# Performance work log

Measured on AMD Instinct MI355X. Metric: run time of the kernel, lower is better.

The kernel has to match this reference:

```python
import jax, jax.numpy as jnp
import numpy as np

N_NODES = 50000
N_EDGES = 800000
IN_DIM, HID_DIM, OUT_DIM, N_HEADS = 256, 256, 64, 4

def setup_inputs() -> dict:
    key = jax.random.key(0)
    ks = jax.random.split(key, 8)
    x = jax.random.normal(ks[0], (N_NODES, IN_DIM), dtype=jnp.float32)
    idx = jax.random.randint(ks[1], (2, N_EDGES), 0, N_NODES, dtype=jnp.int64)
    elem = jax.random.uniform(ks[2], (N_EDGES,), dtype=jnp.float32)
    # MLP params (2 layers: in->hid, hid->out), one set per head; small scale for stability
    W1 = jax.random.normal(ks[3], (N_HEADS, IN_DIM, HID_DIM), dtype=jnp.float32) * 0.05
    b1 = jnp.zeros((N_HEADS, HID_DIM), dtype=jnp.float32)
    W2 = jax.random.normal(ks[4], (N_HEADS, HID_DIM, OUT_DIM), dtype=jnp.float32) * 0.05
    b2 = jnp.zeros((N_HEADS, OUT_DIM), dtype=jnp.float32)
    # Attention: Linear(2*out+1 -> 1)
    attn_w = jax.random.normal(ks[5], (N_HEADS, 2 * OUT_DIM + 1, 1), dtype=jnp.float32) * 0.05
    attn_b = jnp.zeros((N_HEADS, 1), dtype=jnp.float32)
    return {"x": x, "idx": idx, "elem": elem, "W1": W1, "b1": b1,
            "W2": W2, "b2": b2, "attn_w": attn_w, "attn_b": attn_b}

def reference(x, idx, elem, W1, b1, W2, b2, attn_w, attn_b):
    n = x.shape[0]
    src, dst = idx[0], idx[1]

    def head(W1h, b1h, W2h, b2h, awh, abh):
        # 2-layer MLP on node features: [N, out]
        feats = jnp.maximum(x @ W1h + b1h, 0.0) @ W2h + b2h
        f_src = feats[src]            # [E, out]
        f_dst = feats[dst]            # [E, out]
        x_cat = jnp.concatenate([f_src, f_dst, elem[:, None]], axis=1)  # [E, 2*out+1]
        score = (x_cat @ awh + abh)[:, 0]                # [E]
        w = jnp.exp(score - jnp.max(score))              # globally-shifted exp, as in source
        # SpecialSpmm: sparse [N,N] (rows=src, cols=dst, vals=w) @ dense
        pooled = jax.ops.segment_sum(w[:, None] * f_dst, src, num_segments=n)  # [N, out]
        row_sum = jax.ops.segment_sum(w, src, num_segments=n)                  # [N]
        return pooled / row_sum[:, None]

    h = jax.vmap(head)(W1, b1, W2, b2, attn_w, attn_b)   # [H, N, out]
    return jnp.transpose(h, (1, 0, 2)).reshape(n, -1)    # cat heads -> [N, H*out]
```

## Files before the change

kernel.cpp:

```cpp
#include <hip/hip_runtime.h>
#include <math.h>


#define N_HEADS 4
#define IN_DIM 256
#define HID_DIM 256
#define OUT_DIM 64
#define ATT_STRIDE (2 * OUT_DIM + 1)
#define LDSP 264

typedef __attribute__((ext_vector_type(8))) short bf16x8;
typedef __attribute__((ext_vector_type(4))) float f32x4;

__device__ __forceinline__ unsigned short bf16rne(float f) {
  unsigned int u = __float_as_uint(f);
  u += 0x7fffu + ((u >> 16) & 1u);
  return (unsigned short)(u >> 16);
}


#define W1N (N_HEADS * IN_DIM * HID_DIM)
#define W2N (N_HEADS * HID_DIM * OUT_DIM)

__global__ __launch_bounds__(256) void convw_kernel(const float* __restrict__ W1,
                                                    const float* __restrict__ W2,
                                                    unsigned short* __restrict__ W1T,
                                                    unsigned short* __restrict__ W2T) {
  int id = blockIdx.x * 256 + threadIdx.x;
  if (id < W1N) {
    int k = id & 255, j = (id >> 8) & 255, h = id >> 16;
    W1T[id] = bf16rne(W1[((size_t)h * 256 + k) * 256 + j]);
  } else if (id < W1N + W2N) {
    int t = id - W1N;
    int k = t & 255, d = (t >> 8) & 63, h = t >> 14;
    W2T[t] = bf16rne(W2[((size_t)h * 256 + k) * 64 + d]);
  }
}


__global__ __launch_bounds__(256) void count_kernel(const int* __restrict__ src,
                                                    int* __restrict__ cnt, int E) {
  int e = blockIdx.x * 256 + threadIdx.x;
  if (e < E) atomicAdd(&cnt[src[e]], 1);
}

__global__ __launch_bounds__(1024) void scan_kernel(const int* __restrict__ cnt,
                                                    int* __restrict__ offs, int N) {
  __shared__ int part[1024];
  int t = threadIdx.x;
  int chunk = (N + 1023) >> 10;
  int s0 = t * chunk;
  int s1e = min(s0 + chunk, N);
  int sum = 0;
  for (int i = s0; i < s1e; ++i) sum += cnt[i];
  part[t] = sum;
  __syncthreads();
  for (int off = 1; off < 1024; off <<= 1) {
    int v = (t >= off) ? part[t - off] : 0;
    __syncthreads();
    part[t] += v;
    __syncthreads();
  }
  int run = (t == 0) ? 0 : part[t - 1];
  for (int i = s0; i < s1e; ++i) { offs[i] = run; run += cnt[i]; }
  if (t == 0) offs[N] = part[1023];
}

__global__ __launch_bounds__(256) void scatter_kernel(
    const int* __restrict__ src, const int* __restrict__ dst,
    const float* __restrict__ elem, const int* __restrict__ offs,
    int* __restrict__ cur, int* __restrict__ dst2, float* __restrict__ elem2,
    int E) {
  int e = blockIdx.x * 256 + threadIdx.x;
  if (e < E) {
    int s = src[e];
    int pos = offs[s] + atomicAdd(&cur[s], 1);
    dst2[pos] = dst[e];
    elem2[pos] = elem[e];
  }
}


__global__ __launch_bounds__(256) void feats_kernel(
    const float* __restrict__ x, const unsigned short* __restrict__ W1T,
    const float* __restrict__ b1, const unsigned short* __restrict__ W2T,
    const float* __restrict__ b2, const float* __restrict__ attn_w,
    const float* __restrict__ attn_b, unsigned short* __restrict__ feats_g,
    float* __restrict__ s1p, float* __restrict__ s2p, int N) {
  __shared__ __align__(16) unsigned short xs[64 * LDSP];
  __shared__ __align__(16) unsigned short hs[64 * LDSP];

  int n0 = blockIdx.x * 64;
  int tid = threadIdx.x;
  int w = tid >> 6, l = tid & 63;
  int lr = l & 15, kb = l >> 4;

#pragma unroll
  for (int i = 0; i < 8; ++i) {
    int flat = i * 2048 + tid * 8;
    int r = flat >> 8, c = flat & 255;
    int n = n0 + r;
    float4 v0 = make_float4(0.f, 0.f, 0.f, 0.f), v1 = v0;
    if (n < N) {
      const float* p = x + (size_t)n * IN_DIM + c;
      v0 = *(const float4*)p;
      v1 = *(const float4*)(p + 4);
    }
    uint4 pk;
    pk.x = (unsigned)bf16rne(v0.x) | ((unsigned)bf16rne(v0.y) << 16);
    pk.y = (unsigned)bf16rne(v0.z) | ((unsigned)bf16rne(v0.w) << 16);
    pk.z = (unsigned)bf16rne(v1.x) | ((unsigned)bf16rne(v1.y) << 16);
    pk.w = (unsigned)bf16rne(v1.z) | ((unsigned)bf16rne(v1.w) << 16);
    *(uint4*)&xs[r * LDSP + c] = pk;
  }
  __syncthreads();

  int j0 = w * 64;
  for (int h = 0; h < N_HEADS; ++h) {
    const unsigned short* W1Th = W1T + (size_t)h * 256 * 256;
    f32x4 acc[4][4];
#pragma unroll
    for (int mi = 0; mi < 4; ++mi)
#pragma unroll
      for (int ni = 0; ni < 4; ++ni) acc[mi][ni] = (f32x4){0.f, 0.f, 0.f, 0.f};

#pragma unroll
    for (int kk = 0; kk < 8; ++kk) {
      int k0 = kk * 32 + kb * 8;
      bf16x8 a[4], b[4];
#pragma unroll
      for (int mi = 0; mi < 4; ++mi)
        a[mi] = *(const bf16x8*)&xs[(mi * 16 + lr) * LDSP + k0];
#pragma unroll
      for (int ni = 0; ni < 4; ++ni)
        b[ni] = *(const bf16x8*)(W1Th + (size_t)(j0 + ni * 16 + lr) * 256 + k0);
#pragma unroll
      for (int mi = 0; mi < 4; ++mi)
#pragma unroll
        for (int ni = 0; ni < 4; ++ni)
          acc[mi][ni] = __builtin_amdgcn_mfma_f32_16x16x32_bf16(a[mi], b[ni],
                                                                acc[mi][ni], 0, 0, 0);
    }

    float b1v[4];
#pragma unroll
    for (int ni = 0; ni < 4; ++ni) b1v[ni] = b1[h * HID_DIM + j0 + ni * 16 + lr];
    __syncthreads();
#pragma unroll
    for (int mi = 0; mi < 4; ++mi)
#pragma unroll
      for (int ni = 0; ni < 4; ++ni)
#pragma unroll
        for (int r = 0; r < 4; ++r) {
          float v = fmaxf(acc[mi][ni][r] + b1v[ni], 0.0f);
          hs[(mi * 16 + kb * 4 + r) * LDSP + (j0 + ni * 16 + lr)] = bf16rne(v);
        }
    __syncthreads();

    const unsigned short* W2Th = W2T + (size_t)h * 64 * 256;
    f32x4 acc2[4];
#pragma unroll
    for (int ni = 0; ni < 4; ++ni) acc2[ni] = (f32x4){0.f, 0.f, 0.f, 0.f};
#pragma unroll
    for (int kk = 0; kk < 8; ++kk) {
      int k0 = kk * 32 + kb * 8;
      bf16x8 a = *(const bf16x8*)&hs[(w * 16 + lr) * LDSP + k0];
#pragma unroll
      for (int ni = 0; ni < 4; ++ni) {
        bf16x8 b = *(const bf16x8*)(W2Th + (size_t)(ni * 16 + lr) * 256 + k0);
        acc2[ni] = __builtin_amdgcn_mfma_f32_16x16x32_bf16(a, b, acc2[ni], 0, 0, 0);
      }
    }

    const float* awh = attn_w + h * ATT_STRIDE;
    float a1v[4], a2v[4], b2v[4];
#pragma unroll
    for (int ni = 0; ni < 4; ++ni) {
      int d = ni * 16 + lr;
      a1v[ni] = awh[d];
      a2v[ni] = awh[OUT_DIM + d];
      b2v[ni] = b2[h * OUT_DIM + d];
    }
#pragma unroll
    for (int r = 0; r < 4; ++r) {
      int n = n0 + w * 16 + kb * 4 + r;
      float vals[4];
      float p1 = 0.f, p2 = 0.f;
#pragma unroll
      for (int ni = 0; ni < 4; ++ni) {
        float v = acc2[ni][r] + b2v[ni];
        vals[ni] = v;
        p1 += v * a1v[ni];
        p2 += v * a2v[ni];
      }
#pragma unroll
      for (int m = 1; m < 16; m <<= 1) {
        p1 += __shfl_xor(p1, m, 64);
        p2 += __shfl_xor(p2, m, 64);
      }
      if (n < N) {
        unsigned short* fr = feats_g + ((size_t)h * N + n) * OUT_DIM;
#pragma unroll
        for (int ni = 0; ni < 4; ++ni) fr[ni * 16 + lr] = bf16rne(vals[ni]);
        if (lr == 0) {
          s1p[(size_t)n * N_HEADS + h] = p1;
          s2p[(size_t)n * N_HEADS + h] = p2;
        }
      }
    }
  }
}


#define AGG_U 8

__global__ __launch_bounds__(256) void aggregate_kernel(
    const int* __restrict__ dst2, const float* __restrict__ elem2,
    const int* __restrict__ offs, const float* __restrict__ s1p,
    const float* __restrict__ s2p, const unsigned short* __restrict__ feats_g,
    const float* __restrict__ attn_w, const float* __restrict__ attn_b,
    float* __restrict__ out, int N) {
  int n = blockIdx.x;
  int h = threadIdx.x >> 6;
  int l = threadIdx.x & 63;
  int j = l >> 5, dp = l & 31;
  int beg = offs[n], end = offs[n + 1];
  float base = s1p[(size_t)n * N_HEADS + h] + attn_b[h];
  float awe = attn_w[h * ATT_STRIDE + 2 * OUT_DIM];
  const unsigned short* fg = feats_g + (size_t)h * N * OUT_DIM;
  float acc0 = 0.f, acc1 = 0.f, rs = 0.f;

  for (int p = beg; p < end; p += 2 * AGG_U) {
    int dn[AGG_U];
    float el[AGG_U];
#pragma unroll
    for (int i = 0; i < AGG_U; ++i) {
      int q = p + 2 * i + j;
      int qq = (q < end) ? q : beg;
      dn[i] = dst2[qq];
      el[i] = elem2[qq];
    }
    float s2v[AGG_U];
    unsigned int fv[AGG_U];
#pragma unroll
    for (int i = 0; i < AGG_U; ++i) s2v[i] = s2p[(size_t)dn[i] * N_HEADS + h];
#pragma unroll
    for (int i = 0; i < AGG_U; ++i)
      fv[i] = *(const unsigned int*)&fg[(size_t)dn[i] * OUT_DIM + 2 * dp];
#pragma unroll
    for (int i = 0; i < AGG_U; ++i) {
      float wv = (p + 2 * i + j < end) ? __expf(base + s2v[i] + awe * el[i]) : 0.f;
      float f0 = __uint_as_float(fv[i] << 16);
      float f1 = __uint_as_float(fv[i] & 0xffff0000u);
      acc0 = fmaf(wv, f0, acc0);
      acc1 = fmaf(wv, f1, acc1);
      rs += wv;
    }
  }
  acc0 += __shfl_xor(acc0, 32, 64);
  acc1 += __shfl_xor(acc1, 32, 64);
  rs += __shfl_xor(rs, 32, 64);
  if (j == 0) {
    float inv = 1.0f / rs;
    float2 o = make_float2(acc0 * inv, acc1 * inv);
    *(float2*)&out[(size_t)n * (N_HEADS * OUT_DIM) + h * OUT_DIM + 2 * dp] = o;
  }
}


extern "C" void kernel_launch(void* const* d_in, const int* in_sizes, int n_in,
                              void* d_out, int out_size, void* d_ws, size_t ws_size,
                              hipStream_t stream) {
  const float* x = (const float*)d_in[0];
  const int* idx = (const int*)d_in[1];
  const float* elem = (const float*)d_in[2];
  const float* W1 = (const float*)d_in[3];
  const float* b1 = (const float*)d_in[4];
  const float* W2 = (const float*)d_in[5];
  const float* b2 = (const float*)d_in[6];
  const float* attn_w = (const float*)d_in[7];
  const float* attn_b = (const float*)d_in[8];
  float* out = (float*)d_out;

  int N = in_sizes[0] / IN_DIM;
  int E = in_sizes[2];
  const int* src = idx;
  const int* dst = idx + E;
  int nb = (E + 255) / 256;

  unsigned short* W1T = (unsigned short*)d_ws;
  unsigned short* W2T = W1T + W1N;
  unsigned short* feats_g = W2T + W2N;
  float* s1p = (float*)(feats_g + (size_t)N_HEADS * N * OUT_DIM);
  float* s2p = s1p + (size_t)N * N_HEADS;
  int* offs = (int*)(s2p + (size_t)N * N_HEADS);
  int* cur = offs + (N + 64);
  int* dst2 = cur + (N + 64);
  float* elem2 = (float*)(dst2 + E);

  convw_kernel<<<(W1N + W2N + 255) / 256, 256, 0, stream>>>(W1, W2, W1T, W2T);

  hipMemsetAsync(cur, 0, sizeof(int) * (size_t)N, stream);
  count_kernel<<<nb, 256, 0, stream>>>(src, cur, E);
  scan_kernel<<<1, 1024, 0, stream>>>(cur, offs, N);
  hipMemsetAsync(cur, 0, sizeof(int) * (size_t)N, stream);
  scatter_kernel<<<nb, 256, 0, stream>>>(src, dst, elem, offs, cur, dst2, elem2, E);

  feats_kernel<<<(N + 63) / 64, 256, 0, stream>>>(x, W1T, b1, W2T, b2, attn_w,
                                                  attn_b, feats_g, s1p, s2p, N);
  aggregate_kernel<<<N, 256, 0, stream>>>(dst2, elem2, offs, s1p, s2p, feats_g,
                                          attn_w, attn_b, out, N);
}
```

Baseline: 499.9 us.

## Halve feats_kernel row tile and repartition second GEMM across waves

Shrinks the feats_kernel node tile from 64 to 32 rows, halving LDS and accumulator registers, and adds a launch-bounds occupancy hint of 4 blocks. The second GEMM is re-split so each wave owns 16 output columns for all 32 rows, not 16 rows for all columns. Attention dot partials are therefore reduced across waves through shared memory with an extra barrier. The aim is more resident waves and twice as many blocks to hide global W1/W2 loads, at the cost of reloading the weights per smaller tile and extra synchronisation.

```diff
diff --git a/kernel.cpp b/kernel.cpp
--- a/kernel.cpp
+++ b/kernel.cpp
@@ -81,22 +81,23 @@
 }
 
 
-__global__ __launch_bounds__(256) void feats_kernel(
+__global__ __launch_bounds__(256, 4) void feats_kernel(
     const float* __restrict__ x, const unsigned short* __restrict__ W1T,
     const float* __restrict__ b1, const unsigned short* __restrict__ W2T,
     const float* __restrict__ b2, const float* __restrict__ attn_w,
     const float* __restrict__ attn_b, unsigned short* __restrict__ feats_g,
     float* __restrict__ s1p, float* __restrict__ s2p, int N) {
-  __shared__ __align__(16) unsigned short xs[64 * LDSP];
-  __shared__ __align__(16) unsigned short hs[64 * LDSP];
-
-  int n0 = blockIdx.x * 64;
+  __shared__ __align__(16) unsigned short xs[32 * LDSP];
+  __shared__ __align__(16) unsigned short hs[32 * LDSP];
+  __shared__ float part1[32][4], part2[32][4];
+
+  int n0 = blockIdx.x * 32;
   int tid = threadIdx.x;
   int w = tid >> 6, l = tid & 63;
   int lr = l & 15, kb = l >> 4;
 
 #pragma unroll
-  for (int i = 0; i < 8; ++i) {
+  for (int i = 0; i < 4; ++i) {
     int flat = i * 2048 + tid * 8;
     int r = flat >> 8, c = flat & 255;
     int n = n0 + r;
@@ -118,24 +119,24 @@
   int j0 = w * 64;
   for (int h = 0; h < N_HEADS; ++h) {
     const unsigned short* W1Th = W1T + (size_t)h * 256 * 256;
-    f32x4 acc[4][4];
-#pragma unroll
-    for (int mi = 0; mi < 4; ++mi)
+    f32x4 acc[2][4];
+#pragma unroll
+    for (int mi = 0; mi < 2; ++mi)
 #pragma unroll
       for (int ni = 0; ni < 4; ++ni) acc[mi][ni] = (f32x4){0.f, 0.f, 0.f, 0.f};
 
 #pragma unroll
     for (int kk = 0; kk < 8; ++kk) {
       int k0 = kk * 32 + kb * 8;
-      bf16x8 a[4], b[4];
-#pragma unroll
-      for (int mi = 0; mi < 4; ++mi)
+      bf16x8 a[2], b[4];
+#pragma unroll
+      for (int mi = 0; mi < 2; ++mi)
         a[mi] = *(const bf16x8*)&xs[(mi * 16 + lr) * LDSP + k0];
 #pragma unroll
       for (int ni = 0; ni < 4; ++ni)
         b[ni] = *(const bf16x8*)(W1Th + (size_t)(j0 + ni * 16 + lr) * 256 + k0);
 #pragma unroll
-      for (int mi = 0; mi < 4; ++mi)
+      for (int mi = 0; mi < 2; ++mi)
 #pragma unroll
         for (int ni = 0; ni < 4; ++ni)
           acc[mi][ni] = __builtin_amdgcn_mfma_f32_16x16x32_bf16(a[mi], b[ni],
@@ -147,7 +148,7 @@
     for (int ni = 0; ni < 4; ++ni) b1v[ni] = b1[h * HID_DIM + j0 + ni * 16 + lr];
     __syncthreads();
 #pragma unroll
-    for (int mi = 0; mi < 4; ++mi)
+    for (int mi = 0; mi < 2; ++mi)
 #pragma unroll
       for (int ni = 0; ni < 4; ++ni)
 #pragma unroll
@@ -158,54 +159,50 @@
     __syncthreads();
 
     const unsigned short* W2Th = W2T + (size_t)h * 64 * 256;
-    f32x4 acc2[4];
-#pragma unroll
-    for (int ni = 0; ni < 4; ++ni) acc2[ni] = (f32x4){0.f, 0.f, 0.f, 0.f};
+    f32x4 acc2[2];
+#pragma unroll
+    for (int mi = 0; mi < 2; ++mi) acc2[mi] = (f32x4){0.f, 0.f, 0.f, 0.f};
 #pragma unroll
     for (int kk = 0; kk < 8; ++kk) {
       int k0 = kk * 32 + kb * 8;
-      bf16x8 a = *(const bf16x8*)&hs[(w * 16 + lr) * LDSP + k0];
-#pragma unroll
-      for (int ni = 0; ni < 4; ++ni) {
-        bf16x8 b = *(const bf16x8*)(W2Th + (size_t)(ni * 16 + lr) * 256 + k0);
-        acc2[ni] = __builtin_amdgcn_mfma_f32_16x16x32_bf16(a, b, acc2[ni], 0, 0, 0);
+      bf16x8 bfr = *(const bf16x8*)(W2Th + (size_t)(w * 16 + lr) * 256 + k0);
+#pragma unroll
+      for (int mi = 0; mi < 2; ++mi) {
+        bf16x8 a = *(const bf16x8*)&hs[(mi * 16 + lr) * LDSP + k0];
+        acc2[mi] = __builtin_amdgcn_mfma_f32_16x16x32_bf16(a, bfr, acc2[mi], 0, 0, 0);
       }
     }
 
     const float* awh = attn_w + h * ATT_STRIDE;
-    float a1v[4], a2v[4], b2v[4];
-#pragma unroll
-    for (int ni = 0; ni < 4; ++ni) {
-      int d = ni * 16 + lr;
-      a1v[ni] = awh[d];
-      a2v[ni] = awh[OUT_DIM + d];
-      b2v[ni] = b2[h * OUT_DIM + d];
-    }
-#pragma unroll
-    for (int r = 0; r < 4; ++r) {
-      int n = n0 + w * 16 + kb * 4 + r;
-      float vals[4];
-      float p1 = 0.f, p2 = 0.f;
-#pragma unroll
-      for (int ni = 0; ni < 4; ++ni) {
-        float v = acc2[ni][r] + b2v[ni];
-        vals[ni] = v;
-        p1 += v * a1v[ni];
-        p2 += v * a2v[ni];
+    int d = w * 16 + lr;
+    float a1 = awh[d], a2c = awh[OUT_DIM + d], b2d = b2[h * OUT_DIM + d];
+#pragma unroll
+    for (int mi = 0; mi < 2; ++mi)
+#pragma unroll
+      for (int r = 0; r < 4; ++r) {
+        float v = acc2[mi][r] + b2d;
+        int row = mi * 16 + kb * 4 + r;
+        int n = n0 + row;
+        if (n < N) feats_g[((size_t)h * N + n) * OUT_DIM + d] = bf16rne(v);
+        float p1 = v * a1, p2 = v * a2c;
+#pragma unroll
+        for (int m = 1; m < 16; m <<= 1) {
+          p1 += __shfl_xor(p1, m, 64);
+          p2 += __shfl_xor(p2, m, 64);
+        }
+        if (lr == 0) {
+          part1[row][w] = p1;
+          part2[row][w] = p2;
+        }
       }
-#pragma unroll
-      for (int m = 1; m < 16; m <<= 1) {
-        p1 += __shfl_xor(p1, m, 64);
-        p2 += __shfl_xor(p2, m, 64);
-      }
+    __syncthreads();
+    if (tid < 32) {
+      int n = n0 + tid;
       if (n < N) {
-        unsigned short* fr = feats_g + ((size_t)h * N + n) * OUT_DIM;
-#pragma unroll
-        for (int ni = 0; ni < 4; ++ni) fr[ni * 16 + lr] = bf16rne(vals[ni]);
-        if (lr == 0) {
-          s1p[(size_t)n * N_HEADS + h] = p1;
-          s2p[(size_t)n * N_HEADS + h] = p2;
-        }
+        float q1 = part1[tid][0] + part1[tid][1] + part1[tid][2] + part1[tid][3];
+        float q2 = part2[tid][0] + part2[tid][1] + part2[tid][2] + part2[tid][3];
+        s1p[(size_t)n * N_HEADS + h] = q1;
+        s2p[(size_t)n * N_HEADS + h] = q2;
       }
     }
   }
@@ -306,7 +303,7 @@
   hipMemsetAsync(cur, 0, sizeof(int) * (size_t)N, stream);
   scatter_kernel<<<nb, 256, 0, stream>>>(src, dst, elem, offs, cur, dst2, elem2, E);
 
-  feats_kernel<<<(N + 63) / 64, 256, 0, stream>>>(x, W1T, b1, W2T, b2, attn_w,
+  feats_kernel<<<(N + 31) / 32, 256, 0, stream>>>(x, W1T, b1, W2T, b2, attn_w,
                                                   attn_b, feats_g, s1p, s2p, N);
   aggregate_kernel<<<N, 256, 0, stream>>>(dst2, elem2, offs, s1p, s2p, feats_g,
                                           attn_w, attn_b, out, N);
```

New measurement: 509.2 us. Within noise of the previous version (+1.9%).
